# Performance work log

Measured on AMD Instinct MI355X. Metric: run time of the kernel, lower is better.

## Reference

```python
import jax, jax.numpy as jnp
import numpy as np

MARGIN = 0.5

def _pairwise_dist(x):
    # Euclidean cdist with grad-safe sqrt (diagonal is exactly zero).
    sq = jnp.sum(x * x, axis=1)
    d2 = sq[:, None] + sq[None, :] - 2.0 * (x @ x.T)
    d2 = jnp.maximum(d2, 0.0)
    safe = jnp.where(d2 > 0.0, d2, 1.0)
    return jnp.where(d2 > 0.0, jnp.sqrt(safe), 0.0)

def setup_inputs() -> dict:
    key = jax.random.key(0)
    k1, k2 = jax.random.split(key)
    embeddings = jax.random.normal(k1, (8192, 128), dtype=jnp.float32)
    labels = jax.random.randint(k2, (8192,), 0, 256, dtype=jnp.int64)
    return {"embeddings": embeddings, "labels": labels}

def reference(embeddings, labels):
    B = embeddings.shape[0]
    dist = _pairwise_dist(embeddings)                      # [B, B]
    same = labels[:, None] == labels[None, :]              # [B, B]
    eye = jnp.eye(B, dtype=bool)
    pos_mask = same & ~eye
    neg_mask = ~same
    neg_inf = jnp.float32(-jnp.inf)
    pos_inf = jnp.float32(jnp.inf)
    hardest_pos = jnp.max(jnp.where(pos_mask, dist, neg_inf), axis=1)  # [B]
    hardest_neg = jnp.min(jnp.where(neg_mask, dist, pos_inf), axis=1)  # [B]
    valid = jnp.any(pos_mask, axis=1) & jnp.any(neg_mask, axis=1)      # [B]
    per_anchor = jnp.maximum(hardest_pos - hardest_neg + MARGIN, 0.0)
    per_anchor = jnp.where(valid, per_anchor, 0.0)
    num = jnp.sum(valid.astype(jnp.float32))
    return jnp.sum(per_anchor) / jnp.maximum(num, 1.0)
```

## Files before the change

### kernel.cpp

```cpp
#include <hip/hip_runtime.h>
#include <hip/hip_bf16.h>
#include <stdint.h>


typedef __bf16 bf16x8 __attribute__((ext_vector_type(8)));
typedef float f32x4 __attribute__((ext_vector_type(4)));

constexpr int NB = 8192;
constexpr int ND = 128;
constexpr int BM = 256;
constexpr int BN = 64;
constexpr int SPLIT = 16;
constexpr int JRANGE = NB / SPLIT;
constexpr int NT = JRANGE / BN;

constexpr size_t OFF_XB  = 0;
constexpr size_t OFF_SQ  = (size_t)NB * ND * 2;
constexpr size_t OFF_LAB = OFF_SQ + (size_t)NB * 4;
constexpr size_t OFF_HP  = OFF_LAB + (size_t)NB * 4;
constexpr size_t OFF_HN  = OFF_HP + (size_t)SPLIT * NB * 4;
constexpr size_t OFF_ACC = OFF_HN + (size_t)SPLIT * NB * 4;

__device__ __forceinline__ unsigned short f2bf(float f) {
  union { float f; uint32_t u; } c; c.f = f;
  uint32_t u = c.u;
  u += 0x7fffu + ((u >> 16) & 1u);
  return (unsigned short)(u >> 16);
}

__global__ __launch_bounds__(256) void prep_kernel(
    const float* __restrict__ x, const int* __restrict__ labels,
    unsigned short* __restrict__ xb, float* __restrict__ sq,
    int* __restrict__ lab, float* __restrict__ acc, int* __restrict__ cnt) {
  if (blockIdx.x == 0 && threadIdx.x == 0) {
    acc[0] = 0.f;
    acc[1] = 0.f;
    *cnt = 0;
  }
  const int row = blockIdx.x * 8 + (threadIdx.x >> 5);
  const int sub = threadIdx.x & 31;
  const float4 v = *reinterpret_cast<const float4*>(x + (size_t)row * ND + sub * 4);
  ushort4 o;
  o.x = f2bf(v.x); o.y = f2bf(v.y); o.z = f2bf(v.z); o.w = f2bf(v.w);
  *reinterpret_cast<ushort4*>(xb + (size_t)row * ND + sub * 4) = o;
  float s = v.x * v.x + v.y * v.y + v.z * v.z + v.w * v.w;
#pragma unroll
  for (int m = 1; m < 32; m <<= 1) s += __shfl_xor(s, m);
  if (sub == 0) {
    sq[row] = s;
    lab[row] = labels[row];
  }
}

__global__ __launch_bounds__(256, 2) void hard_kernel(
    const unsigned short* __restrict__ xb, const float* __restrict__ sq,
    const int* __restrict__ lab, float* __restrict__ hp_out,
    float* __restrict__ hn_out) {
  __shared__ __align__(16) char smem[2][BN * ND * 2];
  __shared__ float sql[JRANGE];
  __shared__ int labl[JRANGE];
  const int tid = threadIdx.x;
  const int lane = tid & 63;
  const int w = tid >> 6;
  const int rowbase = blockIdx.x * BM;
  const int jbase0 = blockIdx.y * JRANGE;

  const int c16 = lane & 15;
  const int g4 = lane >> 4;

  auto stage = [&](int buf, int tile) {
    const char* gbase = reinterpret_cast<const char*>(xb) +
                        ((size_t)(jbase0 + tile * BN)) * (ND * 2);
#pragma unroll
    for (int rnd = 0; rnd < 4; ++rnd) {
      const int L = rnd * 4096 + tid * 16;
      const int slot = (L >> 4) & 15;
      const int col = L >> 8;
      const int src = (L & ~0xF0) | ((slot ^ (col & 15)) << 4);
      __builtin_amdgcn_global_load_lds(
          (const __attribute__((address_space(1))) unsigned int*)(gbase + src),
          (__attribute__((address_space(3))) unsigned int*)(&smem[buf][L]),
          16, 0, 0);
    }
  };

  stage(0, 0);
  {
    const int i2 = tid * 2;
    *reinterpret_cast<float2*>(&sql[i2]) =
        *reinterpret_cast<const float2*>(&sq[jbase0 + i2]);
    *reinterpret_cast<int2*>(&labl[i2]) =
        *reinterpret_cast<const int2*>(&lab[jbase0 + i2]);
  }

  bf16x8 afrag[4][4];
#pragma unroll
  for (int rt = 0; rt < 4; ++rt) {
    const unsigned short* ap =
        xb + ((size_t)(rowbase + w * 64 + rt * 16 + c16)) * ND + g4 * 8;
#pragma unroll
    for (int kk = 0; kk < 4; ++kk)
      afrag[rt][kk] = *reinterpret_cast<const bf16x8*>(ap + kk * 32);
  }
  int labr[4][4];
#pragma unroll
  for (int rt = 0; rt < 4; ++rt)
#pragma unroll
    for (int r = 0; r < 4; ++r)
      labr[rt][r] = lab[rowbase + w * 64 + rt * 16 + g4 * 4 + r];

  float hp2[4][4], hn2[4][4];
#pragma unroll
  for (int rt = 0; rt < 4; ++rt)
#pragma unroll
    for (int r = 0; r < 4; ++r) {
      hp2[rt][r] = -__builtin_inff();
      hn2[rt][r] = __builtin_inff();
    }

  __syncthreads();

  for (int t = 0; t < NT; ++t) {
    if (t + 1 < NT) stage((t + 1) & 1, t + 1);
    const char* sb = smem[t & 1];
#pragma unroll
    for (int jj = 0; jj < 4; ++jj) {
      const int jidx = t * BN + jj * 16 + c16;
      const float sqc = sql[jidx];
      const int labc = labl[jidx];
      const int colL = jj * 16 + c16;

      bf16x8 bfrag[4];
#pragma unroll
      for (int kk = 0; kk < 4; ++kk) {
        const int kbyte = kk * 64 + g4 * 16;
        const int a = colL * 256 + (kbyte ^ (c16 << 4));
        bfrag[kk] = *reinterpret_cast<const bf16x8*>(sb + a);
      }

      f32x4 acc[4];
#pragma unroll
      for (int rt = 0; rt < 4; ++rt) acc[rt] = (f32x4){0.f, 0.f, 0.f, 0.f};
#pragma unroll
      for (int kk = 0; kk < 4; ++kk)
#pragma unroll
        for (int rt = 0; rt < 4; ++rt)
          acc[rt] = __builtin_amdgcn_mfma_f32_16x16x32_bf16(
              afrag[rt][kk], bfrag[kk], acc[rt], 0, 0, 0);

#pragma unroll
      for (int rt = 0; rt < 4; ++rt)
#pragma unroll
        for (int r = 0; r < 4; ++r) {
          const float tv = fmaf(-2.f, acc[rt][r], sqc);
          const bool same = (labc == labr[rt][r]);
          hp2[rt][r] = fmaxf(hp2[rt][r], same ? tv : -__builtin_inff());
          hn2[rt][r] = fminf(hn2[rt][r], same ? __builtin_inff() : tv);
        }
    }
    __syncthreads();
  }

#pragma unroll
  for (int rt = 0; rt < 4; ++rt)
#pragma unroll
    for (int r = 0; r < 4; ++r) {
      float p = hp2[rt][r], n = hn2[rt][r];
#pragma unroll
      for (int m = 1; m <= 8; m <<= 1) {
        p = fmaxf(p, __shfl_xor(p, m));
        n = fminf(n, __shfl_xor(n, m));
      }
      if (c16 == 0) {
        const int rg = rowbase + w * 64 + rt * 16 + g4 * 4 + r;
        hp_out[(size_t)blockIdx.y * NB + rg] = p;
        hn_out[(size_t)blockIdx.y * NB + rg] = n;
      }
    }
}

__global__ __launch_bounds__(256) void reduce_kernel(
    const float* __restrict__ hp, const float* __restrict__ hn,
    const float* __restrict__ sq, float* __restrict__ acc,
    int* __restrict__ cnt_done, float* __restrict__ out) {
  const int a = blockIdx.x * 256 + threadIdx.x;
  float p = -__builtin_inff(), n = __builtin_inff();
#pragma unroll
  for (int s = 0; s < SPLIT; ++s) {
    p = fmaxf(p, hp[(size_t)s * NB + a]);
    n = fminf(n, hn[(size_t)s * NB + a]);
  }
  const float sqa = sq[a];
  const float d2p = fmaxf(sqa + p, 0.f);
  const float d2n = fmaxf(sqa + n, 0.f);
  const bool valid = (d2p > 1.0f) && (n < 1e37f);
  float loss = valid ? fmaxf(sqrtf(d2p) - sqrtf(d2n) + 0.5f, 0.f) : 0.f;
  float c = valid ? 1.f : 0.f;
#pragma unroll
  for (int m = 1; m < 64; m <<= 1) {
    loss += __shfl_xor(loss, m);
    c += __shfl_xor(c, m);
  }
  __shared__ float ls[4], cs[4];
  const int w = threadIdx.x >> 6, lane = threadIdx.x & 63;
  if (lane == 0) { ls[w] = loss; cs[w] = c; }
  __syncthreads();
  if (threadIdx.x == 0) {
    atomicAdd(&acc[0], ls[0] + ls[1] + ls[2] + ls[3]);
    atomicAdd(&acc[1], cs[0] + cs[1] + cs[2] + cs[3]);
    __threadfence();
    const int old = atomicAdd(cnt_done, 1);
    if (old == (NB / 256) - 1) {
      const float l = atomicAdd(&acc[0], 0.0f);
      const float nvalid = atomicAdd(&acc[1], 0.0f);
      out[0] = l / fmaxf(nvalid, 1.f);
    }
  }
}

extern "C" void kernel_launch(void* const* d_in, const int* in_sizes, int n_in,
                              void* d_out, int out_size, void* d_ws,
                              size_t ws_size, hipStream_t stream) {
  const float* x = (const float*)d_in[0];
  const int* labels = (const int*)d_in[1];
  char* ws = (char*)d_ws;
  unsigned short* xb = (unsigned short*)(ws + OFF_XB);
  float* sq = (float*)(ws + OFF_SQ);
  int* lab = (int*)(ws + OFF_LAB);
  float* hp = (float*)(ws + OFF_HP);
  float* hn = (float*)(ws + OFF_HN);
  float* acc = (float*)(ws + OFF_ACC);
  int* cnt = (int*)(ws + OFF_ACC + 8);

  prep_kernel<<<NB / 8, 256, 0, stream>>>(x, labels, xb, sq, lab, acc, cnt);
  hard_kernel<<<dim3(NB / BM, SPLIT), 256, 0, stream>>>(xb, sq, lab, hp, hn);
  reduce_kernel<<<NB / 256, 256, 0, stream>>>(hp, hn, sq, acc, cnt,
                                              (float*)d_out);
}
```

Measured before the change: 89.65 us.

## Exploit distance matrix symmetry by computing only upper-triangular tile pairs

Replaces the full row-by-column-split sweep with one block per upper-triangular 128x128 tile pair. Each dot product tile now updates both the row anchors' and the column anchors' hardest positive/negative, roughly halving the MFMA work. Row and column partial results go to 2*NTILE slots, so the reduce kernel reads 128 slots instead of 16 and workspace grows. The cost is single-tile blocks with no pipelining, extra epilogue compares, and more launched blocks with heavier per-block setup.

```diff
diff --git a/kernel.cpp b/kernel.cpp
--- a/kernel.cpp
+++ b/kernel.cpp
@@ -8,18 +8,17 @@
 
 constexpr int NB = 8192;
 constexpr int ND = 128;
-constexpr int BM = 256;
-constexpr int BN = 64;
-constexpr int SPLIT = 16;
-constexpr int JRANGE = NB / SPLIT;
-constexpr int NT = JRANGE / BN;
+constexpr int TS = 128;
+constexpr int NTILE = NB / TS;
+constexpr int NPAIR = NTILE * (NTILE + 1) / 2;
+constexpr int SLOTS = 2 * NTILE;
 
 constexpr size_t OFF_XB  = 0;
 constexpr size_t OFF_SQ  = (size_t)NB * ND * 2;
 constexpr size_t OFF_LAB = OFF_SQ + (size_t)NB * 4;
 constexpr size_t OFF_HP  = OFF_LAB + (size_t)NB * 4;
-constexpr size_t OFF_HN  = OFF_HP + (size_t)SPLIT * NB * 4;
-constexpr size_t OFF_ACC = OFF_HN + (size_t)SPLIT * NB * 4;
+constexpr size_t OFF_HN  = OFF_HP + (size_t)SLOTS * NB * 4;
+constexpr size_t OFF_ACC = OFF_HN + (size_t)SLOTS * NB * 4;
 
 __device__ __forceinline__ unsigned short f2bf(float f) {
   union { float f; uint32_t u; } c; c.f = f;
@@ -56,127 +55,155 @@
     const unsigned short* __restrict__ xb, const float* __restrict__ sq,
     const int* __restrict__ lab, float* __restrict__ hp_out,
     float* __restrict__ hn_out) {
-  __shared__ __align__(16) char smem[2][BN * ND * 2];
-  __shared__ float sql[JRANGE];
-  __shared__ int labl[JRANGE];
+  __shared__ __align__(16) char smem[TS * ND * 2];
+  __shared__ float sql[TS];
+  __shared__ int labl[TS];
   const int tid = threadIdx.x;
   const int lane = tid & 63;
   const int w = tid >> 6;
-  const int rowbase = blockIdx.x * BM;
-  const int jbase0 = blockIdx.y * JRANGE;
-
+  const int wr = w >> 1, wc = w & 1;
   const int c16 = lane & 15;
   const int g4 = lane >> 4;
 
-  auto stage = [&](int buf, int tile) {
+  const int q = (NPAIR - 1) - (int)blockIdx.x;
+  int r = (int)((sqrtf(8.f * (float)q + 1.f) - 1.f) * 0.5f);
+  while ((r + 1) * (r + 2) / 2 <= q) ++r;
+  while (r * (r + 1) / 2 > q) --r;
+  const int I = (NTILE - 1) - r;
+  const int J = (NTILE - 1) - (q - r * (r + 1) / 2);
+  const int rowbase = I * TS;
+  const int colbase = J * TS;
+
+  {
     const char* gbase = reinterpret_cast<const char*>(xb) +
-                        ((size_t)(jbase0 + tile * BN)) * (ND * 2);
-#pragma unroll
-    for (int rnd = 0; rnd < 4; ++rnd) {
+                        (size_t)colbase * (ND * 2);
+#pragma unroll
+    for (int rnd = 0; rnd < 8; ++rnd) {
       const int L = rnd * 4096 + tid * 16;
       const int slot = (L >> 4) & 15;
       const int col = L >> 8;
       const int src = (L & ~0xF0) | ((slot ^ (col & 15)) << 4);
       __builtin_amdgcn_global_load_lds(
           (const __attribute__((address_space(1))) unsigned int*)(gbase + src),
-          (__attribute__((address_space(3))) unsigned int*)(&smem[buf][L]),
+          (__attribute__((address_space(3))) unsigned int*)(&smem[L]),
           16, 0, 0);
     }
-  };
-
-  stage(0, 0);
-  {
-    const int i2 = tid * 2;
-    *reinterpret_cast<float2*>(&sql[i2]) =
-        *reinterpret_cast<const float2*>(&sq[jbase0 + i2]);
-    *reinterpret_cast<int2*>(&labl[i2]) =
-        *reinterpret_cast<const int2*>(&lab[jbase0 + i2]);
+  }
+  if (tid < TS) {
+    sql[tid] = sq[colbase + tid];
+    labl[tid] = lab[colbase + tid];
   }
 
   bf16x8 afrag[4][4];
 #pragma unroll
   for (int rt = 0; rt < 4; ++rt) {
     const unsigned short* ap =
-        xb + ((size_t)(rowbase + w * 64 + rt * 16 + c16)) * ND + g4 * 8;
+        xb + ((size_t)(rowbase + wr * 64 + rt * 16 + c16)) * ND + g4 * 8;
 #pragma unroll
     for (int kk = 0; kk < 4; ++kk)
       afrag[rt][kk] = *reinterpret_cast<const bf16x8*>(ap + kk * 32);
   }
   int labr[4][4];
+  float sqr[4][4];
 #pragma unroll
   for (int rt = 0; rt < 4; ++rt)
 #pragma unroll
-    for (int r = 0; r < 4; ++r)
-      labr[rt][r] = lab[rowbase + w * 64 + rt * 16 + g4 * 4 + r];
+    for (int rr = 0; rr < 4; ++rr) {
+      const int rg = rowbase + wr * 64 + rt * 16 + g4 * 4 + rr;
+      labr[rt][rr] = lab[rg];
+      sqr[rt][rr] = sq[rg];
+    }
 
   float hp2[4][4], hn2[4][4];
 #pragma unroll
   for (int rt = 0; rt < 4; ++rt)
 #pragma unroll
-    for (int r = 0; r < 4; ++r) {
-      hp2[rt][r] = -__builtin_inff();
-      hn2[rt][r] = __builtin_inff();
-    }
+    for (int rr = 0; rr < 4; ++rr) {
+      hp2[rt][rr] = -__builtin_inff();
+      hn2[rt][rr] = __builtin_inff();
+    }
+  float cp[4], cn[4];
+#pragma unroll
+  for (int jj = 0; jj < 4; ++jj) {
+    cp[jj] = -__builtin_inff();
+    cn[jj] = __builtin_inff();
+  }
 
   __syncthreads();
 
-  for (int t = 0; t < NT; ++t) {
-    if (t + 1 < NT) stage((t + 1) & 1, t + 1);
-    const char* sb = smem[t & 1];
-#pragma unroll
-    for (int jj = 0; jj < 4; ++jj) {
-      const int jidx = t * BN + jj * 16 + c16;
-      const float sqc = sql[jidx];
-      const int labc = labl[jidx];
-      const int colL = jj * 16 + c16;
-
-      bf16x8 bfrag[4];
-#pragma unroll
-      for (int kk = 0; kk < 4; ++kk) {
-        const int kbyte = kk * 64 + g4 * 16;
-        const int a = colL * 256 + (kbyte ^ (c16 << 4));
-        bfrag[kk] = *reinterpret_cast<const bf16x8*>(sb + a);
-      }
-
-      f32x4 acc[4];
-#pragma unroll
-      for (int rt = 0; rt < 4; ++rt) acc[rt] = (f32x4){0.f, 0.f, 0.f, 0.f};
-#pragma unroll
-      for (int kk = 0; kk < 4; ++kk)
-#pragma unroll
-        for (int rt = 0; rt < 4; ++rt)
-          acc[rt] = __builtin_amdgcn_mfma_f32_16x16x32_bf16(
-              afrag[rt][kk], bfrag[kk], acc[rt], 0, 0, 0);
-
+#pragma unroll
+  for (int jj = 0; jj < 4; ++jj) {
+    const int colL = wc * 64 + jj * 16 + c16;
+    const float sqc = sql[colL];
+    const int labc = labl[colL];
+
+    bf16x8 bfrag[4];
+#pragma unroll
+    for (int kk = 0; kk < 4; ++kk) {
+      const int kbyte = kk * 64 + g4 * 16;
+      const int a = colL * 256 + (kbyte ^ (c16 << 4));
+      bfrag[kk] = *reinterpret_cast<const bf16x8*>(smem + a);
+    }
+
+    f32x4 acc[4];
+#pragma unroll
+    for (int rt = 0; rt < 4; ++rt) acc[rt] = (f32x4){0.f, 0.f, 0.f, 0.f};
+#pragma unroll
+    for (int kk = 0; kk < 4; ++kk)
 #pragma unroll
       for (int rt = 0; rt < 4; ++rt)
-#pragma unroll
-        for (int r = 0; r < 4; ++r) {
-          const float tv = fmaf(-2.f, acc[rt][r], sqc);
-          const bool same = (labc == labr[rt][r]);
-          hp2[rt][r] = fmaxf(hp2[rt][r], same ? tv : -__builtin_inff());
-          hn2[rt][r] = fminf(hn2[rt][r], same ? __builtin_inff() : tv);
-        }
-    }
-    __syncthreads();
-  }
-
+        acc[rt] = __builtin_amdgcn_mfma_f32_16x16x32_bf16(
+            afrag[rt][kk], bfrag[kk], acc[rt], 0, 0, 0);
+
+#pragma unroll
+    for (int rt = 0; rt < 4; ++rt)
+#pragma unroll
+      for (int rr = 0; rr < 4; ++rr) {
+        const float d = acc[rt][rr];
+        const bool same = (labc == labr[rt][rr]);
+        const float tv = fmaf(-2.f, d, sqc);
+        hp2[rt][rr] = fmaxf(hp2[rt][rr], same ? tv : -__builtin_inff());
+        hn2[rt][rr] = fminf(hn2[rt][rr], same ? __builtin_inff() : tv);
+        const float tv2 = fmaf(-2.f, d, sqr[rt][rr]);
+        cp[jj] = fmaxf(cp[jj], same ? tv2 : -__builtin_inff());
+        cn[jj] = fminf(cn[jj], same ? __builtin_inff() : tv2);
+      }
+  }
+
+  const int slotR = 2 * J + wc;
 #pragma unroll
   for (int rt = 0; rt < 4; ++rt)
 #pragma unroll
-    for (int r = 0; r < 4; ++r) {
-      float p = hp2[rt][r], n = hn2[rt][r];
+    for (int rr = 0; rr < 4; ++rr) {
+      float p = hp2[rt][rr], n = hn2[rt][rr];
 #pragma unroll
       for (int m = 1; m <= 8; m <<= 1) {
         p = fmaxf(p, __shfl_xor(p, m));
         n = fminf(n, __shfl_xor(n, m));
       }
       if (c16 == 0) {
-        const int rg = rowbase + w * 64 + rt * 16 + g4 * 4 + r;
-        hp_out[(size_t)blockIdx.y * NB + rg] = p;
-        hn_out[(size_t)blockIdx.y * NB + rg] = n;
-      }
-    }
+        const int rg = rowbase + wr * 64 + rt * 16 + g4 * 4 + rr;
+        hp_out[(size_t)slotR * NB + rg] = p;
+        hn_out[(size_t)slotR * NB + rg] = n;
+      }
+    }
+
+  if (I != J) {
+    const int slotC = 2 * I + wr;
+#pragma unroll
+    for (int jj = 0; jj < 4; ++jj) {
+      float p = cp[jj], n = cn[jj];
+      p = fmaxf(p, __shfl_xor(p, 16));
+      n = fminf(n, __shfl_xor(n, 16));
+      p = fmaxf(p, __shfl_xor(p, 32));
+      n = fminf(n, __shfl_xor(n, 32));
+      if (g4 == 0) {
+        const int cg = colbase + wc * 64 + jj * 16 + c16;
+        hp_out[(size_t)slotC * NB + cg] = p;
+        hn_out[(size_t)slotC * NB + cg] = n;
+      }
+    }
+  }
 }
 
 __global__ __launch_bounds__(256) void reduce_kernel(
@@ -185,8 +212,8 @@
     int* __restrict__ cnt_done, float* __restrict__ out) {
   const int a = blockIdx.x * 256 + threadIdx.x;
   float p = -__builtin_inff(), n = __builtin_inff();
-#pragma unroll
-  for (int s = 0; s < SPLIT; ++s) {
+#pragma unroll 8
+  for (int s = 0; s < SLOTS; ++s) {
     p = fmaxf(p, hp[(size_t)s * NB + a]);
     n = fminf(n, hn[(size_t)s * NB + a]);
   }
@@ -233,7 +260,7 @@
   int* cnt = (int*)(ws + OFF_ACC + 8);
 
   prep_kernel<<<NB / 8, 256, 0, stream>>>(x, labels, xb, sq, lab, acc, cnt);
-  hard_kernel<<<dim3(NB / BM, SPLIT), 256, 0, stream>>>(xb, sq, lab, hp, hn);
+  hard_kernel<<<NPAIR, 256, 0, stream>>>(xb, sq, lab, hp, hn);
   reduce_kernel<<<NB / 256, 256, 0, stream>>>(hp, hn, sq, acc, cnt,
                                               (float*)d_out);
 }
```

Result: slower. 116.7 us (+30.1%).

## Drop LDS staging of column tiles and load B fragments directly from global

Applied to the files above, without the earlier changes.

Removes the double-buffered global_load_lds staging of column tiles and the per-tile barriers. Each wave now reads its B fragments straight from global memory (L2/L1) for every 16-column step. Rows per block drop from 256 to 128 (32 per wave), which doubles the grid and raises the occupancy hint. The cost is more redundant global and L2 traffic, since the column data is no longer shared across waves through LDS. Each B load also now waits on global latency with less compute per fragment to hide it.

```diff
diff --git a/kernel.cpp b/kernel.cpp
--- a/kernel.cpp
+++ b/kernel.cpp
@@ -8,11 +8,10 @@
 
 constexpr int NB = 8192;
 constexpr int ND = 128;
-constexpr int BM = 256;
-constexpr int BN = 64;
 constexpr int SPLIT = 16;
-constexpr int JRANGE = NB / SPLIT;
-constexpr int NT = JRANGE / BN;
+constexpr int JR = NB / SPLIT;
+constexpr int RPB = 128;
+constexpr int NRB = NB / RPB;
 
 constexpr size_t OFF_XB  = 0;
 constexpr size_t OFF_SQ  = (size_t)NB * ND * 2;
@@ -52,127 +51,100 @@
   }
 }
 
-__global__ __launch_bounds__(256, 2) void hard_kernel(
+__global__ __launch_bounds__(256, 4) void hard_kernel(
     const unsigned short* __restrict__ xb, const float* __restrict__ sq,
     const int* __restrict__ lab, float* __restrict__ hp_out,
     float* __restrict__ hn_out) {
-  __shared__ __align__(16) char smem[2][BN * ND * 2];
-  __shared__ float sql[JRANGE];
-  __shared__ int labl[JRANGE];
+  __shared__ float sql[JR];
+  __shared__ int labl[JR];
   const int tid = threadIdx.x;
   const int lane = tid & 63;
   const int w = tid >> 6;
-  const int rowbase = blockIdx.x * BM;
-  const int jbase0 = blockIdx.y * JRANGE;
-
   const int c16 = lane & 15;
   const int g4 = lane >> 4;
-
-  auto stage = [&](int buf, int tile) {
-    const char* gbase = reinterpret_cast<const char*>(xb) +
-                        ((size_t)(jbase0 + tile * BN)) * (ND * 2);
-#pragma unroll
-    for (int rnd = 0; rnd < 4; ++rnd) {
-      const int L = rnd * 4096 + tid * 16;
-      const int slot = (L >> 4) & 15;
-      const int col = L >> 8;
-      const int src = (L & ~0xF0) | ((slot ^ (col & 15)) << 4);
-      __builtin_amdgcn_global_load_lds(
-          (const __attribute__((address_space(1))) unsigned int*)(gbase + src),
-          (__attribute__((address_space(3))) unsigned int*)(&smem[buf][L]),
-          16, 0, 0);
-    }
-  };
-
-  stage(0, 0);
+  const int rowbase = blockIdx.x * RPB + w * 32;
+  const int colbase = blockIdx.y * JR;
+
   {
     const int i2 = tid * 2;
     *reinterpret_cast<float2*>(&sql[i2]) =
-        *reinterpret_cast<const float2*>(&sq[jbase0 + i2]);
+        *reinterpret_cast<const float2*>(&sq[colbase + i2]);
     *reinterpret_cast<int2*>(&labl[i2]) =
-        *reinterpret_cast<const int2*>(&lab[jbase0 + i2]);
-  }
-
-  bf16x8 afrag[4][4];
-#pragma unroll
-  for (int rt = 0; rt < 4; ++rt) {
+        *reinterpret_cast<const int2*>(&lab[colbase + i2]);
+  }
+
+  bf16x8 afrag[2][4];
+#pragma unroll
+  for (int rt = 0; rt < 2; ++rt) {
     const unsigned short* ap =
-        xb + ((size_t)(rowbase + w * 64 + rt * 16 + c16)) * ND + g4 * 8;
+        xb + ((size_t)(rowbase + rt * 16 + c16)) * ND + g4 * 8;
 #pragma unroll
     for (int kk = 0; kk < 4; ++kk)
       afrag[rt][kk] = *reinterpret_cast<const bf16x8*>(ap + kk * 32);
   }
-  int labr[4][4];
-#pragma unroll
-  for (int rt = 0; rt < 4; ++rt)
-#pragma unroll
-    for (int r = 0; r < 4; ++r)
-      labr[rt][r] = lab[rowbase + w * 64 + rt * 16 + g4 * 4 + r];
-
-  float hp2[4][4], hn2[4][4];
-#pragma unroll
-  for (int rt = 0; rt < 4; ++rt)
-#pragma unroll
-    for (int r = 0; r < 4; ++r) {
-      hp2[rt][r] = -__builtin_inff();
-      hn2[rt][r] = __builtin_inff();
+  int labr[2][4];
+#pragma unroll
+  for (int rt = 0; rt < 2; ++rt)
+#pragma unroll
+    for (int rr = 0; rr < 4; ++rr)
+      labr[rt][rr] = lab[rowbase + rt * 16 + g4 * 4 + rr];
+
+  float hp2[2][4], hn2[2][4];
+#pragma unroll
+  for (int rt = 0; rt < 2; ++rt)
+#pragma unroll
+    for (int rr = 0; rr < 4; ++rr) {
+      hp2[rt][rr] = -__builtin_inff();
+      hn2[rt][rr] = __builtin_inff();
     }
 
   __syncthreads();
 
-  for (int t = 0; t < NT; ++t) {
-    if (t + 1 < NT) stage((t + 1) & 1, t + 1);
-    const char* sb = smem[t & 1];
-#pragma unroll
-    for (int jj = 0; jj < 4; ++jj) {
-      const int jidx = t * BN + jj * 16 + c16;
-      const float sqc = sql[jidx];
-      const int labc = labl[jidx];
-      const int colL = jj * 16 + c16;
-
-      bf16x8 bfrag[4];
-#pragma unroll
-      for (int kk = 0; kk < 4; ++kk) {
-        const int kbyte = kk * 64 + g4 * 16;
-        const int a = colL * 256 + (kbyte ^ (c16 << 4));
-        bfrag[kk] = *reinterpret_cast<const bf16x8*>(sb + a);
+#pragma unroll 2
+  for (int jj = 0; jj < JR / 16; ++jj) {
+    const int colL = jj * 16 + c16;
+    const float sqc = sql[colL];
+    const int labc = labl[colL];
+    const unsigned short* bp = xb + (size_t)(colbase + colL) * ND + g4 * 8;
+
+    bf16x8 bfrag[4];
+#pragma unroll
+    for (int kk = 0; kk < 4; ++kk)
+      bfrag[kk] = *reinterpret_cast<const bf16x8*>(bp + kk * 32);
+
+    f32x4 acc[2];
+#pragma unroll
+    for (int rt = 0; rt < 2; ++rt) acc[rt] = (f32x4){0.f, 0.f, 0.f, 0.f};
+#pragma unroll
+    for (int kk = 0; kk < 4; ++kk)
+#pragma unroll
+      for (int rt = 0; rt < 2; ++rt)
+        acc[rt] = __builtin_amdgcn_mfma_f32_16x16x32_bf16(
+            afrag[rt][kk], bfrag[kk], acc[rt], 0, 0, 0);
+
+#pragma unroll
+    for (int rt = 0; rt < 2; ++rt)
+#pragma unroll
+      for (int rr = 0; rr < 4; ++rr) {
+        const float tv = fmaf(-2.f, acc[rt][rr], sqc);
+        const bool same = (labc == labr[rt][rr]);
+        hp2[rt][rr] = fmaxf(hp2[rt][rr], same ? tv : -__builtin_inff());
+        hn2[rt][rr] = fminf(hn2[rt][rr], same ? __builtin_inff() : tv);
       }
-
-      f32x4 acc[4];
-#pragma unroll
-      for (int rt = 0; rt < 4; ++rt) acc[rt] = (f32x4){0.f, 0.f, 0.f, 0.f};
-#pragma unroll
-      for (int kk = 0; kk < 4; ++kk)
-#pragma unroll
-        for (int rt = 0; rt < 4; ++rt)
-          acc[rt] = __builtin_amdgcn_mfma_f32_16x16x32_bf16(
-              afrag[rt][kk], bfrag[kk], acc[rt], 0, 0, 0);
-
-#pragma unroll
-      for (int rt = 0; rt < 4; ++rt)
-#pragma unroll
-        for (int r = 0; r < 4; ++r) {
-          const float tv = fmaf(-2.f, acc[rt][r], sqc);
-          const bool same = (labc == labr[rt][r]);
-          hp2[rt][r] = fmaxf(hp2[rt][r], same ? tv : -__builtin_inff());
-          hn2[rt][r] = fminf(hn2[rt][r], same ? __builtin_inff() : tv);
-        }
-    }
-    __syncthreads();
-  }
-
-#pragma unroll
-  for (int rt = 0; rt < 4; ++rt)
-#pragma unroll
-    for (int r = 0; r < 4; ++r) {
-      float p = hp2[rt][r], n = hn2[rt][r];
+  }
+
+#pragma unroll
+  for (int rt = 0; rt < 2; ++rt)
+#pragma unroll
+    for (int rr = 0; rr < 4; ++rr) {
+      float p = hp2[rt][rr], n = hn2[rt][rr];
 #pragma unroll
       for (int m = 1; m <= 8; m <<= 1) {
         p = fmaxf(p, __shfl_xor(p, m));
         n = fminf(n, __shfl_xor(n, m));
       }
       if (c16 == 0) {
-        const int rg = rowbase + w * 64 + rt * 16 + g4 * 4 + r;
+        const int rg = rowbase + rt * 16 + g4 * 4 + rr;
         hp_out[(size_t)blockIdx.y * NB + rg] = p;
         hn_out[(size_t)blockIdx.y * NB + rg] = n;
       }
@@ -233,7 +205,7 @@
   int* cnt = (int*)(ws + OFF_ACC + 8);
 
   prep_kernel<<<NB / 8, 256, 0, stream>>>(x, labels, xb, sq, lab, acc, cnt);
-  hard_kernel<<<dim3(NB / BM, SPLIT), 256, 0, stream>>>(xb, sq, lab, hp, hn);
+  hard_kernel<<<dim3(NRB, SPLIT), 256, 0, stream>>>(xb, sq, lab, hp, hn);
   reduce_kernel<<<NB / 256, 256, 0, stream>>>(hp, hn, sq, acc, cnt,
                                               (float*)d_out);
 }
```

New measurement: 128.8 us. 1.44x slower.
